# Optimization experiments

Hardware: AMD Instinct MI355X
Metric: run time of the kernel (lower is better)

The kernel has to match this reference:

```python
import math
import jax, jax.numpy as jnp
import numpy as np

B, T, C = 1, 2048, 2048
H, G, D = 16, 4, 128          # n_head, n_query_groups, head_size; C == H*D
Q_PER_KV = H // G
EPS = 1e-5


def _apply_rope_interleaved(x, cos, sin):
    # x: [B, T, h, D]; cos/sin: [T, D//2]; interleaved (GPT-J) style pairs
    x1 = x[..., 0::2]
    x2 = x[..., 1::2]
    c = cos[None, :, None, :]
    s = sin[None, :, None, :]
    o1 = x1 * c - x2 * s
    o2 = x1 * s + x2 * c
    return jnp.stack([o1, o2], axis=-1).reshape(x.shape)


def setup_inputs() -> dict:
    key = jax.random.key(0)
    k0, k1, k2, k3 = jax.random.split(key, 4)
    x = jax.random.normal(k0, (B, T, C), jnp.float32)
    # rotary cache (standard theta=10000)
    inv_freq = 1.0 / (10000.0 ** (np.arange(0, D, 2, dtype=np.float64) / D))
    ang = np.outer(np.arange(T, dtype=np.float64), inv_freq)
    cos = jnp.asarray(np.cos(ang), jnp.float32)
    sin = jnp.asarray(np.sin(ang), jnp.float32)
    # RetNet per-head decay mask: D[h,i,j] = gamma_h^(i-j) for i>=j else 0
    gammas = 1.0 - 2.0 ** (-5.0 - np.arange(H, dtype=np.float64))
    i = np.arange(T)[:, None]
    j = np.arange(T)[None, :]
    diff = np.maximum(i - j, 0).astype(np.float64)
    m = np.where(i >= j, gammas[:, None, None] ** diff[None], 0.0)
    mask = jnp.asarray(m, jnp.float32)
    std = 0.02
    W_reten = jax.random.normal(k1, (C, (H + 2 * G) * D), jnp.float32) * std
    W_gate = jax.random.normal(k2, (C, C), jnp.float32) * std
    W_proj = jax.random.normal(k3, (C, C), jnp.float32) * std
    return {"x": x, "cos": cos, "sin": sin, "mask": mask,
            "W_reten": W_reten, "W_gate": W_gate, "W_proj": W_proj,
            "max_seq_length": T}


def reference(x, cos, sin, mask, W_reten, W_gate, W_proj, max_seq_length):
    # fused qkv projection, grouped-query layout
    qkv = (x @ W_reten).reshape(B, T, G, Q_PER_KV + 2, D)
    q = qkv[..., :Q_PER_KV, :].reshape(B, T, H, D)
    k = qkv[..., Q_PER_KV:Q_PER_KV + 1, :].reshape(B, T, G, D)
    v = qkv[..., Q_PER_KV + 1:, :].reshape(B, T, G, D)
    q = _apply_rope_interleaved(q, cos, sin)
    k = _apply_rope_interleaved(k, cos, sin)
    # [B, h, T, D]
    q = q.transpose(0, 2, 1, 3)
    k = jnp.repeat(k.transpose(0, 2, 1, 3), Q_PER_KV, axis=1)
    v = jnp.repeat(v.transpose(0, 2, 1, 3), Q_PER_KV, axis=1)
    # parallel retention: masked (decay) scores, no softmax
    scale = 1.0 / math.sqrt(D)
    qk = jnp.einsum('bhtd,bhsd->bhts', q, k) * scale
    qk = qk * mask[None]
    y = jnp.einsum('bhts,bhsd->bhtd', qk, v)
    # group norm = RMSNorm (no weight) over head_size
    y = y.transpose(0, 2, 1, 3)  # [B, T, H, D]
    y = y * jax.lax.rsqrt(jnp.mean(y * y, axis=-1, keepdims=True) + EPS)
    y = y.reshape(B, T, C)
    g = jax.nn.silu(x @ W_gate)
    return (g * y) @ W_proj
```

## Files before the change

kernel.cpp:

```cpp
#include <hip/hip_runtime.h>
#include <hip/hip_bf16.h>
#include <cstdint>
#include <cstddef>

typedef __bf16 bf16x8 __attribute__((ext_vector_type(8)));
typedef __bf16 bf16x4 __attribute__((ext_vector_type(4)));
typedef __bf16 bf16x2 __attribute__((ext_vector_type(2)));
typedef float  f32x4  __attribute__((ext_vector_type(4)));
typedef float  f32x2  __attribute__((ext_vector_type(2)));

#define T_SEQ 2048
#define CDIM  2048
#define NH    16
#define NG    4
#define DH    128
#define NCHUNK 32

__device__ __forceinline__ void gl_lds16(const __bf16* g, __bf16* l) {
  __builtin_amdgcn_global_load_lds(
      (const __attribute__((address_space(1))) void*)g,
      (__attribute__((address_space(3))) void*)l, 16, 0, 0);
}

__global__ __launch_bounds__(256) void pre_kernel(
    const float* __restrict__ x, const float* __restrict__ Wr,
    const float* __restrict__ Wg, const float* __restrict__ Wp,
    __bf16* __restrict__ xb, __bf16* __restrict__ wtb, __bf16* __restrict__ wpb) {
  __shared__ __bf16 tile[64][68];
  int bid = blockIdx.x;
  int tid = threadIdx.x;
  if (bid < 2048) {
    size_t i = ((size_t)bid * 256 + tid) * 8;
    f32x4 a = *(const f32x4*)(x + i);
    f32x4 b = *(const f32x4*)(x + i + 4);
    bf16x8 o;
#pragma unroll
    for (int j = 0; j < 4; ++j) { o[j] = (__bf16)a[j]; o[4 + j] = (__bf16)b[j]; }
    *(bf16x8*)(xb + i) = o;
    return;
  }
  int rel = bid - 2048;
  const float* W; __bf16* Wt; int N;
  if (rel < 1536)      { W = Wr; Wt = wtb;                        N = 3072; }
  else if (rel < 2560) { W = Wg; Wt = wtb + (size_t)3072 * CDIM;  N = 2048; rel -= 1536; }
  else                 { W = Wp; Wt = wpb;                        N = 2048; rel -= 2560; }
  const int K = 2048;
  int k0 = (rel & 31) * 64, n0 = (rel >> 5) * 64;
  int c4 = (tid & 15) * 4, r = tid >> 4;
#pragma unroll
  for (int rr = 0; rr < 4; ++rr) {
    int row = r + rr * 16;
    f32x4 v = *(const f32x4*)(W + (size_t)(k0 + row) * N + n0 + c4);
#pragma unroll
    for (int j = 0; j < 4; ++j) tile[row][c4 + j] = (__bf16)v[j];
  }
  __syncthreads();
  int n = tid >> 2, seg = tid & 3;
  __bf16 vals[16];
#pragma unroll
  for (int j = 0; j < 16; ++j) vals[j] = tile[seg * 16 + j][n];
  __bf16* dst = Wt + (size_t)(n0 + n) * K + k0 + seg * 16;
  *(bf16x8*)(dst)     = *(bf16x8*)(&vals[0]);
  *(bf16x8*)(dst + 8) = *(bf16x8*)(&vals[8]);
}

__global__ __launch_bounds__(256) void uscan_kernel(const __bf16* __restrict__ vtb,
                                                    const __bf16* __restrict__ ktb,
                                                    __bf16* __restrict__ St) {
  int bid = blockIdx.x;
  int h = bid >> 4, m = (bid >> 1) & 7, half = bid & 1;
  int g = h >> 2;
  int tid = threadIdx.x, w = tid >> 6, l = tid & 63, lr = l & 15, lg = l >> 4;
  int jf = half * 4 + w;
  float l2g = log2f(1.0f - exp2f(-5.0f - (float)h));
  float ginv = exp2f(-l2g);
  float df   = exp2f(l2g * 64.0f);
  float wk[2];
#pragma unroll
  for (int kk = 0; kk < 2; ++kk) wk[kk] = exp2f(l2g * (float)(64 - (kk * 32 + lg * 8)));
  const __bf16* vrow = vtb + ((size_t)g * DH + m * 16 + lr) * T_SEQ;
  const __bf16* krow = ktb + ((size_t)g * DH + jf * 16 + lr) * T_SEQ;
  f32x4 S = {0.f, 0.f, 0.f, 0.f};
  for (int c = 0; c < NCHUNK; ++c) {
    f32x4 u = {0.f, 0.f, 0.f, 0.f};
#pragma unroll
    for (int kk = 0; kk < 2; ++kk) {
      int j0 = c * 64 + kk * 32 + lg * 8;
      bf16x8 av = *(const bf16x8*)(vrow + j0);
      bf16x8 bv = *(const bf16x8*)(krow + j0);
      bf16x8 aw;
      float wj = wk[kk];
#pragma unroll
      for (int jj = 0; jj < 8; ++jj) { aw[jj] = (__bf16)((float)av[jj] * wj); wj *= ginv; }
      u = __builtin_amdgcn_mfma_f32_16x16x32_bf16(aw, bv, u, 0, 0, 0);
    }
    __bf16* out = St + ((size_t)(h * NCHUNK + c) * 128 + m * 16 + lg * 4) * 128 + jf * 16 + lr;
#pragma unroll
    for (int r = 0; r < 4; ++r) out[r * 128] = (__bf16)S[r];
#pragma unroll
    for (int r = 0; r < 4; ++r) S[r] = df * S[r] + u[r];
  }
}

__global__ __launch_bounds__(256) void attn2_kernel(const __bf16* __restrict__ qb,
    const __bf16* __restrict__ kb, const __bf16* __restrict__ vtb,
    const __bf16* __restrict__ St, const __bf16* __restrict__ gateb,
    __bf16* __restrict__ ynormb) {
  __shared__ __bf16 kl[64 * 128];
  __shared__ __bf16 vl[128 * 64];
  __shared__ __bf16 pl[4][16 * 64];
  int h = blockIdx.x >> 5, qt = blockIdx.x & 31;
  int g = h >> 2;
  int w = threadIdx.x >> 6, l = threadIdx.x & 63;
  int lr = l & 15, lg = l >> 4;
  int t0b = qt * 64;
  int t0 = t0b + w * 16;
  bf16x8 qf[4];
#pragma unroll
  for (int kbk = 0; kbk < 4; ++kbk)
    qf[kbk] = *(const bf16x8*)(qb + ((size_t)h * T_SEQ + t0 + lr) * DH + kbk * 32 + lg * 8);
  float gamma = 1.0f - exp2f(-5.0f - (float)h);
  float l2g = log2f(gamma);
  const float scale = 0.088388347648318447f;
  int s0 = t0b;
#pragma unroll
  for (int it = 0; it < 4; ++it) {
    int fg = it * 256 + threadIdx.x;
    {
      int ss = fg >> 4, gr = fg & 15;
      bf16x8 kv = *(const bf16x8*)(kb + ((size_t)g * T_SEQ + s0 + ss) * DH + gr * 8);
      *(bf16x8*)((char*)kl + ss * 256 + ((gr * 16) ^ ((ss & 7) << 4))) = kv;
    }
    {
      int d = fg >> 3, gv = fg & 7;
      bf16x8 vv = *(const bf16x8*)(vtb + ((size_t)g * DH + d) * T_SEQ + s0 + gv * 8);
      *(bf16x8*)((char*)vl + d * 128 + ((gv * 16) ^ ((d & 7) << 4))) = vv;
    }
  }
  float wfac = scale * exp2f(l2g * (float)(w * 16 + lr));
  bf16x8 qwf[4];
#pragma unroll
  for (int kbk = 0; kbk < 4; ++kbk)
#pragma unroll
    for (int e = 0; e < 8; ++e) qwf[kbk][e] = (__bf16)((float)qf[kbk][e] * wfac);
  f32x4 acc[8] = {};
  const __bf16* Sb = St + (size_t)(h * NCHUNK + qt) * 16384;
#pragma unroll
  for (int dc = 0; dc < 8; ++dc)
#pragma unroll
    for (int kc = 0; kc < 4; ++kc) {
      bf16x8 sf = *(const bf16x8*)(Sb + (dc * 16 + lr) * 128 + kc * 32 + lg * 8);
      acc[dc] = __builtin_amdgcn_mfma_f32_16x16x32_bf16(qwf[kc], sf, acc[dc], 0, 0, 0);
    }
  __syncthreads();
#pragma unroll
  for (int sc = 0; sc < 4; ++sc) {
    f32x4 p = {0.f, 0.f, 0.f, 0.f};
    int srow = sc * 16 + lr;
#pragma unroll
    for (int kbk = 0; kbk < 4; ++kbk) {
      bf16x8 kf = *(const bf16x8*)((char*)kl + srow * 256 +
                                   ((kbk * 64 + lg * 16) ^ ((srow & 7) << 4)));
      p = __builtin_amdgcn_mfma_f32_16x16x32_bf16(qf[kbk], kf, p, 0, 0, 0);
    }
#pragma unroll
    for (int r = 0; r < 4; ++r) {
      int tl = lg * 4 + r;
      int diff = (w * 16 + tl) - srow;
      float val = 0.0f;
      if (diff >= 0) val = p[r] * scale * exp2f((float)diff * l2g);
      *(__bf16*)((char*)(pl[w]) + tl * 128 +
                 (((sc * 16 + lr) * 2) ^ ((tl & 7) << 4))) = (__bf16)val;
    }
  }
  bf16x8 pa[2];
#pragma unroll
  for (int kc = 0; kc < 2; ++kc)
    pa[kc] = *(const bf16x8*)((char*)(pl[w]) + lr * 128 +
                              ((kc * 64 + lg * 16) ^ ((lr & 7) << 4)));
#pragma unroll
  for (int dc = 0; dc < 8; ++dc) {
#pragma unroll
    for (int kc = 0; kc < 2; ++kc) {
      int vrow = dc * 16 + lr;
      bf16x8 vf = *(const bf16x8*)((char*)vl + vrow * 128 +
                                   ((kc * 64 + lg * 16) ^ ((vrow & 7) << 4)));
      acc[dc] = __builtin_amdgcn_mfma_f32_16x16x32_bf16(pa[kc], vf, acc[dc], 0, 0, 0);
    }
  }
  float rs[4];
#pragma unroll
  for (int r = 0; r < 4; ++r) {
    float ssum = 0.f;
#pragma unroll
    for (int dc = 0; dc < 8; ++dc) ssum += acc[dc][r] * acc[dc][r];
    ssum += __shfl_xor(ssum, 1, 64);
    ssum += __shfl_xor(ssum, 2, 64);
    ssum += __shfl_xor(ssum, 4, 64);
    ssum += __shfl_xor(ssum, 8, 64);
    rs[r] = rsqrtf(ssum * (1.0f / 128.0f) + 1e-5f);
  }
#pragma unroll
  for (int dc = 0; dc < 8; ++dc)
#pragma unroll
    for (int r = 0; r < 4; ++r) {
      size_t idx = (size_t)(t0 + lg * 4 + r) * CDIM + h * DH + dc * 16 + lr;
      float gv = (float)gateb[idx];
      ynormb[idx] = (__bf16)(acc[dc][r] * rs[r] * gv);
    }
}

template<int MODE>
__global__ __launch_bounds__(256) void gemm_gl_kernel(
    const __bf16* __restrict__ A, const __bf16* __restrict__ Bt,
    float* __restrict__ Cf, __bf16* __restrict__ Cg,
    const float* __restrict__ cosb, const float* __restrict__ sinb,
    __bf16* __restrict__ qb, __bf16* __restrict__ kb,
    __bf16* __restrict__ vtb, __bf16* __restrict__ ktb,
    int M, int N, int K) {
  __shared__ __bf16 Asb[64 * 64];
  __shared__ __bf16 Bsb[128 * 64];
  int m0 = blockIdx.x * 64, n0 = blockIdx.y * 128;
  int tid = threadIdx.x;
  int w = tid >> 6, l = tid & 63;
  int wr = w >> 1, wc = w & 1;
  int lr = l & 15, lg = l >> 4;
  int nk = K >> 6;
  const __bf16* Ab = A + (size_t)m0 * K;
  const __bf16* Bb = Bt + (size_t)n0 * K;
  f32x4 acc[2][4] = {};
  for (int kt = 0; kt < nk; ++kt) {
    int k0 = kt << 6;
#pragma unroll
    for (int c = 0; c < 2; ++c) {
      int ca = c * 256 + tid;
      int row = ca >> 3, kseg = ca & 7;
      gl_lds16(Ab + (size_t)row * K + k0 + ((kseg ^ (row & 7)) << 3), Asb + ca * 8);
    }
#pragma unroll
    for (int c = 0; c < 4; ++c) {
      int cb = c * 256 + tid;
      int row = cb >> 3, kseg = cb & 7;
      gl_lds16(Bb + (size_t)row * K + k0 + ((kseg ^ (row & 7)) << 3), Bsb + cb * 8);
    }
    __syncthreads();
    bf16x8 av[2][2], bv[4][2];
#pragma unroll
    for (int i = 0; i < 2; ++i)
#pragma unroll
      for (int kk = 0; kk < 2; ++kk) {
        int row = wr * 32 + i * 16 + lr;
        av[i][kk] = *(const bf16x8*)((const char*)Asb +
            ((row * 128 + kk * 64 + lg * 16) ^ ((lr & 7) << 4)));
      }
#pragma unroll
    for (int j = 0; j < 4; ++j)
#pragma unroll
      for (int kk = 0; kk < 2; ++kk) {
        int row = wc * 64 + j * 16 + lr;
        bv[j][kk] = *(const bf16x8*)((const char*)Bsb +
            ((row * 128 + kk * 64 + lg * 16) ^ ((lr & 7) << 4)));
      }
#pragma unroll
    for (int kk = 0; kk < 2; ++kk)
#pragma unroll
      for (int i = 0; i < 2; ++i)
#pragma unroll
        for (int j = 0; j < 4; ++j)
          acc[i][j] = __builtin_amdgcn_mfma_f32_16x16x32_bf16(av[i][kk], bv[j][kk],
                                                              acc[i][j], 0, 0, 0);
    __syncthreads();
  }
  if (MODE == 0) {
#pragma unroll
    for (int i = 0; i < 2; ++i) {
      int row = m0 + wr * 32 + i * 16 + lg * 4;
#pragma unroll
      for (int j = 0; j < 4; ++j) {
        int col = n0 + wc * 64 + j * 16 + lr;
#pragma unroll
        for (int r = 0; r < 4; ++r)
          Cf[(size_t)(row + r) * N + col] = acc[i][j][r];
      }
    }
    return;
  }
  if (n0 >= 3072) {
#pragma unroll
    for (int i = 0; i < 2; ++i) {
      int row = m0 + wr * 32 + i * 16 + lg * 4;
#pragma unroll
      for (int j = 0; j < 4; ++j) {
        int col = n0 + wc * 64 + j * 16 + lr;
#pragma unroll
        for (int r = 0; r < 4; ++r) {
          float z = acc[i][j][r];
          float sv = z / (1.0f + expf(-z));
          Cg[(size_t)(row + r) * 2048 + (col - 3072)] = (__bf16)sv;
        }
      }
    }
    return;
  }
#pragma unroll
  for (int i = 0; i < 2; ++i) {
    int row0 = m0 + wr * 32 + i * 16 + lg * 4;
#pragma unroll
    for (int j = 0; j < 4; ++j) {
      int cb = n0 + wc * 64 + j * 16;
      int g = cb / 768, cm = cb % 768;
      int dbase = (cm < 512) ? (cm & 127) : (cm < 640) ? (cm - 512) : (cm - 640);
      int d = dbase + lr;
      float ov[4];
      if (cm < 640) {
#pragma unroll
        for (int r = 0; r < 4; ++r) {
          float z = acc[i][j][r];
          float pz = __shfl_xor(z, 1, 64);
          int t = row0 + r;
          float cc = cosb[t * 64 + (d >> 1)];
          float ss = sinb[t * 64 + (d >> 1)];
          ov[r] = (lr & 1) ? (pz * ss + z * cc) : (z * cc - pz * ss);
        }
      } else {
#pragma unroll
        for (int r = 0; r < 4; ++r) ov[r] = acc[i][j][r];
      }
      if (cm < 512) {
        int hh = g * 4 + (cm >> 7);
#pragma unroll
        for (int r = 0; r < 4; ++r)
          qb[((size_t)hh * T_SEQ + row0 + r) * DH + d] = (__bf16)ov[r];
      } else if (cm < 640) {
        bf16x4 kv;
#pragma unroll
        for (int r = 0; r < 4; ++r) {
          kv[r] = (__bf16)ov[r];
          kb[((size_t)g * T_SEQ + row0 + r) * DH + d] = kv[r];
        }
        *(bf16x4*)(ktb + ((size_t)g * DH + d) * T_SEQ + row0) = kv;
      } else {
        bf16x4 vv;
#pragma unroll
        for (int r = 0; r < 4; ++r) vv[r] = (__bf16)ov[r];
        *(bf16x4*)(vtb + ((size_t)g * DH + d) * T_SEQ + row0) = vv;
      }
    }
  }
}

extern "C" void kernel_launch(void* const* d_in, const int* in_sizes, int n_in,
                              void* d_out, int out_size, void* d_ws, size_t ws_size,
                              hipStream_t stream) {
  const float* x    = (const float*)d_in[0];
  const float* cosb = (const float*)d_in[1];
  const float* sinb = (const float*)d_in[2];
  const float* Wr   = (const float*)d_in[4];
  const float* Wg   = (const float*)d_in[5];
  const float* Wp   = (const float*)d_in[6];

  char* ws = (char*)d_ws;
  size_t off = 0;
  auto alloc = [&](size_t bytes) { void* p = ws + off; off += (bytes + 255) & ~(size_t)255; return p; };
  __bf16* xb     = (__bf16*)alloc((size_t)CDIM * CDIM * 2);
  __bf16* wtb    = (__bf16*)alloc((size_t)5120 * CDIM * 2);
  __bf16* wpb    = (__bf16*)alloc((size_t)CDIM * CDIM * 2);
  __bf16* qb     = (__bf16*)alloc((size_t)NH * T_SEQ * DH * 2);
  __bf16* kbp    = (__bf16*)alloc((size_t)NG * T_SEQ * DH * 2);
  __bf16* vtb    = (__bf16*)alloc((size_t)NG * DH * T_SEQ * 2);
  __bf16* ktb    = (__bf16*)alloc((size_t)NG * DH * T_SEQ * 2);
  __bf16* gateb  = (__bf16*)alloc((size_t)CDIM * CDIM * 2);
  __bf16* Stb    = (__bf16*)alloc((size_t)NH * NCHUNK * 128 * 128 * 2);
  __bf16* ynormb = (__bf16*)alloc((size_t)T_SEQ * CDIM * 2);

  pre_kernel<<<5632, 256, 0, stream>>>(x, Wr, Wg, Wp, xb, wtb, wpb);
  gemm_gl_kernel<1><<<dim3(32, 40), 256, 0, stream>>>(
      xb, wtb, nullptr, gateb, cosb, sinb, qb, kbp, vtb, ktb, 2048, 5120, 2048);
  uscan_kernel<<<256, 256, 0, stream>>>(vtb, ktb, Stb);
  attn2_kernel<<<NH * NCHUNK, 256, 0, stream>>>(qb, kbp, vtb, Stb, gateb, ynormb);
  gemm_gl_kernel<0><<<dim3(32, 16), 256, 0, stream>>>(
      ynormb, wpb, (float*)d_out, nullptr, nullptr, nullptr, nullptr, nullptr, nullptr, nullptr,
      2048, 2048, 2048);
}
```

Baseline: 164.0 us.

## Double-buffer LDS tiles in GEMM kernel with async global-to-LDS prefetch

Doubles the shared-memory buffers in the templated GEMM and prefetches the tile two k-steps ahead using global_load_lds, with explicit vmcnt waits and raw barriers replacing the load-then-syncthreads loop. The aim is to overlap global memory latency with MFMA compute. It doubles LDS use per block, which may lower occupancy. Correctness depends on the hand-written waitcnt counts matching the six loads issued per stage.

```diff
diff --git a/kernel.cpp b/kernel.cpp
--- a/kernel.cpp
+++ b/kernel.cpp
@@ -218,8 +218,8 @@
     __bf16* __restrict__ qb, __bf16* __restrict__ kb,
     __bf16* __restrict__ vtb, __bf16* __restrict__ ktb,
     int M, int N, int K) {
-  __shared__ __bf16 Asb[64 * 64];
-  __shared__ __bf16 Bsb[128 * 64];
+  __shared__ __bf16 Asb[2 * 64 * 64];
+  __shared__ __bf16 Bsb[2 * 128 * 64];
   int m0 = blockIdx.x * 64, n0 = blockIdx.y * 128;
   int tid = threadIdx.x;
   int w = tid >> 6, l = tid & 63;
@@ -229,28 +229,42 @@
   const __bf16* Ab = A + (size_t)m0 * K;
   const __bf16* Bb = Bt + (size_t)n0 * K;
   f32x4 acc[2][4] = {};
+
+  auto stage = [&](int buf, int k0) {
+#pragma unroll
+    for (int c = 0; c < 2; ++c) {
+      int ca = c * 256 + tid, row = ca >> 3, ks = ca & 7;
+      gl_lds16(Ab + (size_t)row * K + k0 + ((ks ^ (row & 7)) << 3),
+               Asb + buf * 4096 + ca * 8);
+    }
+#pragma unroll
+    for (int c = 0; c < 4; ++c) {
+      int cb2 = c * 256 + tid, row = cb2 >> 3, ks = cb2 & 7;
+      gl_lds16(Bb + (size_t)row * K + k0 + ((ks ^ (row & 7)) << 3),
+               Bsb + buf * 8192 + cb2 * 8);
+    }
+  };
+
+  stage(0, 0);
+  if (nk > 1) {
+    stage(1, 64);
+    asm volatile("s_waitcnt vmcnt(6)" ::: "memory");
+  } else {
+    asm volatile("s_waitcnt vmcnt(0)" ::: "memory");
+  }
+  __builtin_amdgcn_s_barrier();
+
+  int cur = 0;
   for (int kt = 0; kt < nk; ++kt) {
-    int k0 = kt << 6;
-#pragma unroll
-    for (int c = 0; c < 2; ++c) {
-      int ca = c * 256 + tid;
-      int row = ca >> 3, kseg = ca & 7;
-      gl_lds16(Ab + (size_t)row * K + k0 + ((kseg ^ (row & 7)) << 3), Asb + ca * 8);
-    }
-#pragma unroll
-    for (int c = 0; c < 4; ++c) {
-      int cb = c * 256 + tid;
-      int row = cb >> 3, kseg = cb & 7;
-      gl_lds16(Bb + (size_t)row * K + k0 + ((kseg ^ (row & 7)) << 3), Bsb + cb * 8);
-    }
-    __syncthreads();
+    const char* As = (const char*)(Asb + cur * 4096);
+    const char* Bs = (const char*)(Bsb + cur * 8192);
     bf16x8 av[2][2], bv[4][2];
 #pragma unroll
     for (int i = 0; i < 2; ++i)
 #pragma unroll
       for (int kk = 0; kk < 2; ++kk) {
         int row = wr * 32 + i * 16 + lr;
-        av[i][kk] = *(const bf16x8*)((const char*)Asb +
+        av[i][kk] = *(const bf16x8*)(As +
             ((row * 128 + kk * 64 + lg * 16) ^ ((lr & 7) << 4)));
       }
 #pragma unroll
@@ -258,7 +272,7 @@
 #pragma unroll
       for (int kk = 0; kk < 2; ++kk) {
         int row = wc * 64 + j * 16 + lr;
-        bv[j][kk] = *(const bf16x8*)((const char*)Bsb +
+        bv[j][kk] = *(const bf16x8*)(Bs +
             ((row * 128 + kk * 64 + lg * 16) ^ ((lr & 7) << 4)));
       }
 #pragma unroll
@@ -269,8 +283,19 @@
         for (int j = 0; j < 4; ++j)
           acc[i][j] = __builtin_amdgcn_mfma_f32_16x16x32_bf16(av[i][kk], bv[j][kk],
                                                               acc[i][j], 0, 0, 0);
-    __syncthreads();
-  }
+    if (kt + 1 < nk) {
+      __builtin_amdgcn_s_barrier();
+      if (kt + 2 < nk) {
+        stage(cur, (kt + 2) << 6);
+        asm volatile("s_waitcnt vmcnt(6)" ::: "memory");
+      } else {
+        asm volatile("s_waitcnt vmcnt(0)" ::: "memory");
+      }
+      __builtin_amdgcn_s_barrier();
+    }
+    cur ^= 1;
+  }
+
   if (MODE == 0) {
 #pragma unroll
     for (int i = 0; i < 2; ++i) {
```

Result: faster. 156.4 us, median of 2 (-4.6%).
